# Kernel tuning notes

Measured on AMD Instinct MI355X. Metric: run time of the kernel, lower is better.

## Reference

```python
import jax, jax.numpy as jnp
import numpy as np

B, T, H = 32, 2048, 1024


def setup_inputs() -> dict:
    key = jax.random.key(0)
    ks = jax.random.split(key, 5)
    s = 1.0 / np.sqrt(H)
    return {
        "x": jax.random.normal(ks[0], (B, H), dtype=jnp.float32),
        "context": jax.random.normal(ks[1], (B, T, H), dtype=jnp.float32),
        "mask": jnp.ones((B, T), dtype=bool),
        "Wq": jax.random.normal(ks[2], (H, H), dtype=jnp.float32) * s,
        "bq": jnp.zeros((H,), dtype=jnp.float32),
        "Wm": jax.random.normal(ks[3], (H, H), dtype=jnp.float32) * s,
        "bm": jnp.zeros((H,), dtype=jnp.float32),
        "v": jax.random.normal(ks[4], (H,), dtype=jnp.float32) * s,
    }


def reference(x, context, mask, Wq, bq, Wm, bm, v):
    # h_x: [B,1,H]; h_c: [B,T,H]  (mask is unused, matching the original module)
    h_x = (x @ Wq.T + bq)[:, None, :]
    h_c = jnp.einsum('bth,oh->bto', context, Wm) + bm
    # score: [B,T] = tanh(h_x + h_c) . v, then softmax over T
    score = jax.nn.softmax(jnp.einsum('bth,h->bt', jnp.tanh(h_x + h_c), v), axis=-1)
    # context-weighted sum over T -> [B,H]
    c = jnp.einsum('bth,bt->bh', context, score)
    return (c, score)
```

## Files before the change

### kernel.cpp

```cpp
#include <hip/hip_runtime.h>
#include <math.h>

#define B_ 32
#define T_ 2048
#define H_ 1024

typedef __bf16 bf16x8 __attribute__((ext_vector_type(8)));
typedef float f32x4 __attribute__((ext_vector_type(4)));

__device__ __forceinline__ unsigned short f2bf(float f) {
  unsigned int u = __float_as_uint(f);
  u += 0x7fffu + ((u >> 16) & 1u);
  return (unsigned short)(u >> 16);
}

__device__ __forceinline__ float bf2f(unsigned short s) {
  return __uint_as_float(((unsigned int)s) << 16);
}

__device__ __forceinline__ float fast_tanh(float x) {
  float e = __expf(2.0f * x);
  return 1.0f - __fdividef(2.0f, e + 1.0f);
}

__device__ __forceinline__ void async16(const void* g, void* l) {
  typedef const __attribute__((address_space(1))) void* gvp;
  typedef __attribute__((address_space(3))) void* lvp;
  __builtin_amdgcn_global_load_lds((gvp)(unsigned long long)g,
                                   (lvp)(unsigned int)(unsigned long long)l,
                                   16, 0, 0);
}

__global__ void prep_kernel(const float* __restrict__ x, const float* __restrict__ Wq,
                            const float* __restrict__ bq, const float* __restrict__ bm,
                            const float* __restrict__ Wm, const float* __restrict__ ctx,
                            float* __restrict__ hxb, unsigned short* __restrict__ wmb,
                            unsigned short* __restrict__ ctxb,
                            float* __restrict__ logits, float* __restrict__ outc) {
  int blk = blockIdx.x, tid = threadIdx.x;
  if (blk < 8192) {
    int wave = tid >> 6, lane = tid & 63;
    int pair = (blk << 2) + wave;
    int b = pair >> 10, o = pair & (H_ - 1);
    const float4* wr = (const float4*)(Wq + (size_t)o * H_);
    const float4* xr = (const float4*)(x + (size_t)b * H_);
    float s = 0.f;
#pragma unroll
    for (int s4 = 0; s4 < 4; ++s4) {
      float4 wv = wr[(s4 << 6) + lane];
      float4 xv = xr[(s4 << 6) + lane];
      s += wv.x * xv.x + wv.y * xv.y + wv.z * xv.z + wv.w * xv.w;
    }
#pragma unroll
    for (int d = 1; d < 64; d <<= 1) s += __shfl_xor(s, d);
    if (lane == 0) hxb[(b << 10) + o] = s + bq[o] + bm[o];
  } else if (blk < 9216) {
    int i = ((blk - 8192) << 10) + (tid << 2);
    float4 wv = *(const float4*)(Wm + i);
    *(ushort4*)(wmb + i) = make_ushort4(f2bf(wv.x), f2bf(wv.y), f2bf(wv.z), f2bf(wv.w));
  } else if (blk < 9312) {
    int zblk = blk - 9216;
    if (zblk < 64) {
      *(float4*)(logits + (zblk << 10) + (tid << 2)) = (float4){0.f, 0.f, 0.f, 0.f};
    } else {
      *(float4*)(outc + ((zblk - 64) << 10) + (tid << 2)) = (float4){0.f, 0.f, 0.f, 0.f};
    }
  } else {
    size_t i = ((size_t)(blk - 9312) << 11) + ((size_t)tid << 3);
    float4 a = *(const float4*)(ctx + i);
    float4 c = *(const float4*)(ctx + i + 4);
    *(ushort4*)(ctxb + i) = make_ushort4(f2bf(a.x), f2bf(a.y), f2bf(a.z), f2bf(a.w));
    *(ushort4*)(ctxb + i + 4) = make_ushort4(f2bf(c.x), f2bf(c.y), f2bf(c.z), f2bf(c.w));
  }
}

template <bool PRECONV>
__global__ __launch_bounds__(256) void score_kernel(
    const float* __restrict__ ctxf, const unsigned short* __restrict__ ctxb,
    const unsigned short* __restrict__ wmb,
    const float* __restrict__ hxb, const float* __restrict__ v,
    float* logits) {
  __shared__ __align__(16) unsigned short As[128 * 64];
  __shared__ __align__(16) unsigned short Bs[128 * 64];
  __shared__ float part[128];

  int tid = threadIdx.x;
  int xx = blockIdx.x;
  int ot = xx >> 9;
  int bt = xx & 511;
  int b = bt >> 4;
  int t0 = (bt & 15) << 7;
  int o0 = ot << 7;
  if (tid < 128) part[tid] = 0.f;

  int lane = tid & 63;
  int wave = tid >> 6;
  int wm = (wave >> 1) << 6;
  int wn = (wave & 1) << 6;
  int q = lane >> 4;
  int m = lane & 15;

  const unsigned short* cb = PRECONV ? (ctxb + ((size_t)b * T_ + t0) * H_) : nullptr;
  const float* cf = PRECONV ? nullptr : (ctxf + ((size_t)b * T_ + t0) * H_);
  const unsigned short* wb = wmb + (size_t)o0 * H_;

  f32x4 acc[4][4];
#pragma unroll
  for (int i = 0; i < 4; ++i)
#pragma unroll
    for (int j = 0; j < 4; ++j) acc[i][j] = (f32x4){0.f, 0.f, 0.f, 0.f};

  for (int k0 = 0; k0 < H_; k0 += 64) {
    __syncthreads();
#pragma unroll
    for (int i = 0; i < 4; ++i) {
      int ig = (wave << 2) + i;
      int p = (ig << 6) + lane;
      int row = p >> 3;
      int gl = (p & 7) ^ (row & 7);
      size_t goff = (size_t)row * H_ + k0 + (gl << 3);
      if (PRECONV) {
        async16(cb + goff, (char*)As + ((size_t)ig << 10));
      } else {
        int arow = (tid >> 3) + (i << 5);
        int agl = tid & 7;
        int agp = agl ^ (arow & 7);
        const float* src = cf + (size_t)arow * H_ + k0 + (agl << 3);
        float4 f0 = *(const float4*)(src);
        float4 f1 = *(const float4*)(src + 4);
        unsigned short* dst = As + (arow << 6) + (agp << 3);
        *(ushort4*)(dst) = make_ushort4(f2bf(f0.x), f2bf(f0.y), f2bf(f0.z), f2bf(f0.w));
        *(ushort4*)(dst + 4) = make_ushort4(f2bf(f1.x), f2bf(f1.y), f2bf(f1.z), f2bf(f1.w));
      }
      async16(wb + goff, (char*)Bs + ((size_t)ig << 10));
    }
    __syncthreads();
#pragma unroll
    for (int kk = 0; kk < 2; ++kk) {
      bf16x8 af[4], bfr[4];
#pragma unroll
      for (int i = 0; i < 4; ++i) {
        int row = wm + (i << 4) + m;
        int gp = ((kk << 2) + q) ^ (row & 7);
        af[i] = *(const bf16x8*)(As + (row << 6) + (gp << 3));
      }
#pragma unroll
      for (int j = 0; j < 4; ++j) {
        int row = wn + (j << 4) + m;
        int gp = ((kk << 2) + q) ^ (row & 7);
        bfr[j] = *(const bf16x8*)(Bs + (row << 6) + (gp << 3));
      }
#pragma unroll
      for (int i = 0; i < 4; ++i)
#pragma unroll
        for (int j = 0; j < 4; ++j)
          acc[i][j] = __builtin_amdgcn_mfma_f32_16x16x32_bf16(af[i], bfr[j], acc[i][j], 0, 0, 0);
    }
  }

  float hb[4], vv[4];
#pragma unroll
  for (int j = 0; j < 4; ++j) {
    int o = o0 + wn + (j << 4) + m;
    hb[j] = hxb[(b << 10) + o];
    vv[j] = v[o];
  }
#pragma unroll
  for (int i = 0; i < 4; ++i) {
#pragma unroll
    for (int r = 0; r < 4; ++r) {
      float s = 0.f;
#pragma unroll
      for (int j = 0; j < 4; ++j) s += fast_tanh(acc[i][j][r] + hb[j]) * vv[j];
      s += __shfl_xor(s, 1);
      s += __shfl_xor(s, 2);
      s += __shfl_xor(s, 4);
      s += __shfl_xor(s, 8);
      if (m == 0) atomicAdd(&part[wm + (i << 4) + (q << 2) + r], s);
    }
  }
  __syncthreads();
  if (tid < 128) atomicAdd(&logits[b * T_ + t0 + tid], part[tid]);
}

template <bool PRECONV>
__global__ void wsum_kernel(const float* __restrict__ ctxf, const unsigned short* __restrict__ ctxb,
                            const float* __restrict__ logits,
                            float* __restrict__ score, float* __restrict__ outc) {
  int tid = threadIdx.x;
  int b = blockIdx.y;
  int tc = blockIdx.x << 7;
  __shared__ float wred[4];
  __shared__ float sc[128];

  const float* lb = logits + b * T_;
  float l[8];
  float mx = -3.4e38f;
#pragma unroll
  for (int i = 0; i < 8; ++i) { l[i] = lb[tid + (i << 8)]; mx = fmaxf(mx, l[i]); }
#pragma unroll
  for (int d = 1; d < 64; d <<= 1) mx = fmaxf(mx, __shfl_xor(mx, d));
  if ((tid & 63) == 0) wred[tid >> 6] = mx;
  __syncthreads();
  mx = fmaxf(fmaxf(wred[0], wred[1]), fmaxf(wred[2], wred[3]));
  __syncthreads();
  float e[8];
  float se = 0.f;
#pragma unroll
  for (int i = 0; i < 8; ++i) { e[i] = __expf(l[i] - mx); se += e[i]; }
#pragma unroll
  for (int d = 1; d < 64; d <<= 1) se += __shfl_xor(se, d);
  if ((tid & 63) == 0) wred[tid >> 6] = se;
  __syncthreads();
  se = wred[0] + wred[1] + wred[2] + wred[3];
  float inv = 1.0f / se;
#pragma unroll
  for (int i = 0; i < 8; ++i) {
    int tg = tid + (i << 8);
    if ((tg >> 7) == (int)blockIdx.x) sc[tg & 127] = e[i] * inv;
  }
  if (blockIdx.x == 0) {
#pragma unroll
    for (int i = 0; i < 8; ++i) score[b * T_ + tid + (i << 8)] = e[i] * inv;
  }
  __syncthreads();

  int h = tid << 2;
  float s0 = 0.f, s1 = 0.f, s2 = 0.f, s3 = 0.f;
  if (PRECONV) {
    const unsigned short* cp = ctxb + ((size_t)b * T_ + tc) * H_ + h;
#pragma unroll 4
    for (int t = 0; t < 128; ++t) {
      uint2 u = *(const uint2*)(cp + (size_t)t * H_);
      float w = sc[t];
      s0 += bf2f((unsigned short)(u.x & 0xffffu)) * w;
      s1 += bf2f((unsigned short)(u.x >> 16)) * w;
      s2 += bf2f((unsigned short)(u.y & 0xffffu)) * w;
      s3 += bf2f((unsigned short)(u.y >> 16)) * w;
    }
  } else {
    const float* cp = ctxf + ((size_t)b * T_ + tc) * H_ + h;
#pragma unroll 4
    for (int t = 0; t < 128; ++t) {
      float4 f = *(const float4*)(cp + (size_t)t * H_);
      float w = sc[t];
      s0 += f.x * w; s1 += f.y * w; s2 += f.z * w; s3 += f.w * w;
    }
  }
  float* op = outc + (b << 10) + h;
  atomicAdd(op + 0, s0);
  atomicAdd(op + 1, s1);
  atomicAdd(op + 2, s2);
  atomicAdd(op + 3, s3);
}

extern "C" void kernel_launch(void* const* d_in, const int* in_sizes, int n_in,
                              void* d_out, int out_size, void* d_ws, size_t ws_size,
                              hipStream_t stream) {
  const float* x   = (const float*)d_in[0];
  const float* ctx = (const float*)d_in[1];
  const float* Wq  = (const float*)d_in[3];
  const float* bq  = (const float*)d_in[4];
  const float* Wm  = (const float*)d_in[5];
  const float* bm  = (const float*)d_in[6];
  const float* v   = (const float*)d_in[7];

  float* out_c = (float*)d_out;
  float* out_s = out_c + B_ * H_;

  char* ws = (char*)d_ws;
  float* hxb = (float*)ws;
  unsigned short* wmb = (unsigned short*)(ws + 131072);
  float* logits = (float*)(ws + 131072 + 2097152);
  size_t off_ctxb = 131072 + 2097152 + 262144;
  unsigned short* ctxb = (unsigned short*)(ws + off_ctxb);
  size_t need = off_ctxb + (size_t)B_ * T_ * H_ * 2;
  bool preconv = (ws_size >= need);

  int prep_blocks = preconv ? (9312 + 32768) : 9312;
  prep_kernel<<<dim3(prep_blocks), 256, 0, stream>>>(x, Wq, bq, bm, Wm, ctx, hxb, wmb,
                                                     preconv ? ctxb : nullptr, logits, out_c);
  if (preconv) {
    score_kernel<true><<<dim3(4096), 256, 0, stream>>>(ctx, ctxb, wmb, hxb, v, logits);
    wsum_kernel<true><<<dim3(T_ / 128, B_), 256, 0, stream>>>(ctx, ctxb, logits, out_s, out_c);
  } else {
    score_kernel<false><<<dim3(4096), 256, 0, stream>>>(ctx, ctxb, wmb, hxb, v, logits);
    wsum_kernel<false><<<dim3(T_ / 128, B_), 256, 0, stream>>>(ctx, ctxb, logits, out_s, out_c);
  }
}
```

Baseline: 653.8 us.

## Fuse softmax and weighted context sum into the score GEMM kernel

Each score block now loops over all eight 128-wide output chunks itself, so the full logit for its 128 timesteps is ready on-chip. The block then applies an unnormalised exp (without max subtraction) and accumulates the exp-weighted context sum straight away, while its context rows are likely still in cache. Global sums are collected by atomics, and a small finalize kernel divides by the per-batch denominator. This removes the logits round trip, the separate wsum kernel and its cross-block softmax recompute. The hx GEMV also now reuses each Wq row across all batches. In exchange the grid drops from 4096 to 512 blocks, which lowers parallelism and latency hiding, and dropping the max subtraction risks overflow if logits grow large.

```diff
diff --git a/kernel.cpp b/kernel.cpp
--- a/kernel.cpp
+++ b/kernel.cpp
@@ -36,37 +36,39 @@
                             const float* __restrict__ Wm, const float* __restrict__ ctx,
                             float* __restrict__ hxb, unsigned short* __restrict__ wmb,
                             unsigned short* __restrict__ ctxb,
-                            float* __restrict__ logits, float* __restrict__ outc) {
+                            float* __restrict__ den, float* __restrict__ outc) {
   int blk = blockIdx.x, tid = threadIdx.x;
-  if (blk < 8192) {
+  if (blk < 256) {
     int wave = tid >> 6, lane = tid & 63;
-    int pair = (blk << 2) + wave;
-    int b = pair >> 10, o = pair & (H_ - 1);
+    int o = (blk << 2) + wave;
     const float4* wr = (const float4*)(Wq + (size_t)o * H_);
-    const float4* xr = (const float4*)(x + (size_t)b * H_);
-    float s = 0.f;
-#pragma unroll
-    for (int s4 = 0; s4 < 4; ++s4) {
-      float4 wv = wr[(s4 << 6) + lane];
-      float4 xv = xr[(s4 << 6) + lane];
-      s += wv.x * xv.x + wv.y * xv.y + wv.z * xv.z + wv.w * xv.w;
-    }
-#pragma unroll
-    for (int d = 1; d < 64; d <<= 1) s += __shfl_xor(s, d);
-    if (lane == 0) hxb[(b << 10) + o] = s + bq[o] + bm[o];
-  } else if (blk < 9216) {
-    int i = ((blk - 8192) << 10) + (tid << 2);
+    float4 wv[4];
+#pragma unroll
+    for (int s4 = 0; s4 < 4; ++s4) wv[s4] = wr[(s4 << 6) + lane];
+    float bias = bq[o] + bm[o];
+#pragma unroll 4
+    for (int b = 0; b < B_; ++b) {
+      const float4* xr = (const float4*)(x + (size_t)b * H_);
+      float s = 0.f;
+#pragma unroll
+      for (int s4 = 0; s4 < 4; ++s4) {
+        float4 xv = xr[(s4 << 6) + lane];
+        s += wv[s4].x * xv.x + wv[s4].y * xv.y + wv[s4].z * xv.z + wv[s4].w * xv.w;
+      }
+#pragma unroll
+      for (int d = 1; d < 64; d <<= 1) s += __shfl_xor(s, d);
+      if (lane == 0) hxb[(b << 10) + o] = s + bias;
+    }
+  } else if (blk < 1280) {
+    int i = ((blk - 256) << 10) + (tid << 2);
     float4 wv = *(const float4*)(Wm + i);
     *(ushort4*)(wmb + i) = make_ushort4(f2bf(wv.x), f2bf(wv.y), f2bf(wv.z), f2bf(wv.w));
-  } else if (blk < 9312) {
-    int zblk = blk - 9216;
-    if (zblk < 64) {
-      *(float4*)(logits + (zblk << 10) + (tid << 2)) = (float4){0.f, 0.f, 0.f, 0.f};
-    } else {
-      *(float4*)(outc + ((zblk - 64) << 10) + (tid << 2)) = (float4){0.f, 0.f, 0.f, 0.f};
-    }
+  } else if (blk < 1312) {
+    int zb = blk - 1280;
+    *(float4*)(outc + (zb << 10) + (tid << 2)) = (float4){0.f, 0.f, 0.f, 0.f};
+    if (zb == 0 && tid < B_) den[tid] = 0.f;
   } else {
-    size_t i = ((size_t)(blk - 9312) << 11) + ((size_t)tid << 3);
+    size_t i = ((size_t)(blk - 1312) << 11) + ((size_t)tid << 3);
     float4 a = *(const float4*)(ctx + i);
     float4 c = *(const float4*)(ctx + i + 4);
     *(ushort4*)(ctxb + i) = make_ushort4(f2bf(a.x), f2bf(a.y), f2bf(a.z), f2bf(a.w));
@@ -79,18 +81,16 @@
     const float* __restrict__ ctxf, const unsigned short* __restrict__ ctxb,
     const unsigned short* __restrict__ wmb,
     const float* __restrict__ hxb, const float* __restrict__ v,
-    float* logits) {
+    float* __restrict__ outs, float* __restrict__ outc, float* __restrict__ den) {
   __shared__ __align__(16) unsigned short As[128 * 64];
   __shared__ __align__(16) unsigned short Bs[128 * 64];
   __shared__ float part[128];
 
   int tid = threadIdx.x;
-  int xx = blockIdx.x;
-  int ot = xx >> 9;
-  int bt = xx & 511;
-  int b = bt >> 4;
-  int t0 = (bt & 15) << 7;
-  int o0 = ot << 7;
+  int bx = blockIdx.x;
+  int b = bx >> 4;
+  int t0 = (bx & 15) << 7;
+
   if (tid < 128) part[tid] = 0.f;
 
   int lane = tid & 63;
@@ -102,148 +102,120 @@
 
   const unsigned short* cb = PRECONV ? (ctxb + ((size_t)b * T_ + t0) * H_) : nullptr;
   const float* cf = PRECONV ? nullptr : (ctxf + ((size_t)b * T_ + t0) * H_);
-  const unsigned short* wb = wmb + (size_t)o0 * H_;
-
-  f32x4 acc[4][4];
-#pragma unroll
-  for (int i = 0; i < 4; ++i)
-#pragma unroll
-    for (int j = 0; j < 4; ++j) acc[i][j] = (f32x4){0.f, 0.f, 0.f, 0.f};
-
-  for (int k0 = 0; k0 < H_; k0 += 64) {
-    __syncthreads();
+
+  for (int oc = 0; oc < 8; ++oc) {
+    int o0 = oc << 7;
+    const unsigned short* wb = wmb + (size_t)o0 * H_;
+
+    f32x4 acc[4][4];
+#pragma unroll
+    for (int i = 0; i < 4; ++i)
+#pragma unroll
+      for (int j = 0; j < 4; ++j) acc[i][j] = (f32x4){0.f, 0.f, 0.f, 0.f};
+
+    for (int k0 = 0; k0 < H_; k0 += 64) {
+      __syncthreads();
+#pragma unroll
+      for (int i = 0; i < 4; ++i) {
+        int ig = (wave << 2) + i;
+        int p = (ig << 6) + lane;
+        int row = p >> 3;
+        int gl = (p & 7) ^ (row & 7);
+        size_t goff = (size_t)row * H_ + k0 + (gl << 3);
+        if (PRECONV) {
+          async16(cb + goff, (char*)As + ((size_t)ig << 10));
+        } else {
+          int arow = (tid >> 3) + (i << 5);
+          int agl = tid & 7;
+          int agp = agl ^ (arow & 7);
+          const float* src = cf + (size_t)arow * H_ + k0 + (agl << 3);
+          float4 f0 = *(const float4*)(src);
+          float4 f1 = *(const float4*)(src + 4);
+          unsigned short* dst = As + (arow << 6) + (agp << 3);
+          *(ushort4*)(dst) = make_ushort4(f2bf(f0.x), f2bf(f0.y), f2bf(f0.z), f2bf(f0.w));
+          *(ushort4*)(dst + 4) = make_ushort4(f2bf(f1.x), f2bf(f1.y), f2bf(f1.z), f2bf(f1.w));
+        }
+        async16(wb + goff, (char*)Bs + ((size_t)ig << 10));
+      }
+      __syncthreads();
+#pragma unroll
+      for (int kk = 0; kk < 2; ++kk) {
+        bf16x8 af[4], bfr[4];
+#pragma unroll
+        for (int i = 0; i < 4; ++i) {
+          int row = wm + (i << 4) + m;
+          int gp = ((kk << 2) + q) ^ (row & 7);
+          af[i] = *(const bf16x8*)(As + (row << 6) + (gp << 3));
+        }
+#pragma unroll
+        for (int j = 0; j < 4; ++j) {
+          int row = wn + (j << 4) + m;
+          int gp = ((kk << 2) + q) ^ (row & 7);
+          bfr[j] = *(const bf16x8*)(Bs + (row << 6) + (gp << 3));
+        }
+#pragma unroll
+        for (int i = 0; i < 4; ++i)
+#pragma unroll
+          for (int j = 0; j < 4; ++j)
+            acc[i][j] = __builtin_amdgcn_mfma_f32_16x16x32_bf16(af[i], bfr[j], acc[i][j], 0, 0, 0);
+      }
+    }
+
+    float hb[4], vv[4];
+#pragma unroll
+    for (int j = 0; j < 4; ++j) {
+      int o = o0 + wn + (j << 4) + m;
+      hb[j] = hxb[(b << 10) + o];
+      vv[j] = v[o];
+    }
 #pragma unroll
     for (int i = 0; i < 4; ++i) {
-      int ig = (wave << 2) + i;
-      int p = (ig << 6) + lane;
-      int row = p >> 3;
-      int gl = (p & 7) ^ (row & 7);
-      size_t goff = (size_t)row * H_ + k0 + (gl << 3);
-      if (PRECONV) {
-        async16(cb + goff, (char*)As + ((size_t)ig << 10));
-      } else {
-        int arow = (tid >> 3) + (i << 5);
-        int agl = tid & 7;
-        int agp = agl ^ (arow & 7);
-        const float* src = cf + (size_t)arow * H_ + k0 + (agl << 3);
-        float4 f0 = *(const float4*)(src);
-        float4 f1 = *(const float4*)(src + 4);
-        unsigned short* dst = As + (arow << 6) + (agp << 3);
-        *(ushort4*)(dst) = make_ushort4(f2bf(f0.x), f2bf(f0.y), f2bf(f0.z), f2bf(f0.w));
-        *(ushort4*)(dst + 4) = make_ushort4(f2bf(f1.x), f2bf(f1.y), f2bf(f1.z), f2bf(f1.w));
-      }
-      async16(wb + goff, (char*)Bs + ((size_t)ig << 10));
-    }
-    __syncthreads();
-#pragma unroll
-    for (int kk = 0; kk < 2; ++kk) {
-      bf16x8 af[4], bfr[4];
-#pragma unroll
-      for (int i = 0; i < 4; ++i) {
-        int row = wm + (i << 4) + m;
-        int gp = ((kk << 2) + q) ^ (row & 7);
-        af[i] = *(const bf16x8*)(As + (row << 6) + (gp << 3));
-      }
-#pragma unroll
-      for (int j = 0; j < 4; ++j) {
-        int row = wn + (j << 4) + m;
-        int gp = ((kk << 2) + q) ^ (row & 7);
-        bfr[j] = *(const bf16x8*)(Bs + (row << 6) + (gp << 3));
-      }
-#pragma unroll
-      for (int i = 0; i < 4; ++i)
-#pragma unroll
-        for (int j = 0; j < 4; ++j)
-          acc[i][j] = __builtin_amdgcn_mfma_f32_16x16x32_bf16(af[i], bfr[j], acc[i][j], 0, 0, 0);
-    }
-  }
-
-  float hb[4], vv[4];
-#pragma unroll
-  for (int j = 0; j < 4; ++j) {
-    int o = o0 + wn + (j << 4) + m;
-    hb[j] = hxb[(b << 10) + o];
-    vv[j] = v[o];
-  }
-#pragma unroll
-  for (int i = 0; i < 4; ++i) {
-#pragma unroll
-    for (int r = 0; r < 4; ++r) {
-      float s = 0.f;
-#pragma unroll
-      for (int j = 0; j < 4; ++j) s += fast_tanh(acc[i][j][r] + hb[j]) * vv[j];
-      s += __shfl_xor(s, 1);
-      s += __shfl_xor(s, 2);
-      s += __shfl_xor(s, 4);
-      s += __shfl_xor(s, 8);
-      if (m == 0) atomicAdd(&part[wm + (i << 4) + (q << 2) + r], s);
-    }
-  }
+#pragma unroll
+      for (int r = 0; r < 4; ++r) {
+        float s = 0.f;
+#pragma unroll
+        for (int j = 0; j < 4; ++j) s += fast_tanh(acc[i][j][r] + hb[j]) * vv[j];
+        s += __shfl_xor(s, 1);
+        s += __shfl_xor(s, 2);
+        s += __shfl_xor(s, 4);
+        s += __shfl_xor(s, 8);
+        if (m == 0) atomicAdd(&part[wm + (i << 4) + (q << 2) + r], s);
+      }
+    }
+  }
+
   __syncthreads();
-  if (tid < 128) atomicAdd(&logits[b * T_ + t0 + tid], part[tid]);
-}
-
-template <bool PRECONV>
-__global__ void wsum_kernel(const float* __restrict__ ctxf, const unsigned short* __restrict__ ctxb,
-                            const float* __restrict__ logits,
-                            float* __restrict__ score, float* __restrict__ outc) {
-  int tid = threadIdx.x;
-  int b = blockIdx.y;
-  int tc = blockIdx.x << 7;
-  __shared__ float wred[4];
-  __shared__ float sc[128];
-
-  const float* lb = logits + b * T_;
-  float l[8];
-  float mx = -3.4e38f;
-#pragma unroll
-  for (int i = 0; i < 8; ++i) { l[i] = lb[tid + (i << 8)]; mx = fmaxf(mx, l[i]); }
-#pragma unroll
-  for (int d = 1; d < 64; d <<= 1) mx = fmaxf(mx, __shfl_xor(mx, d));
-  if ((tid & 63) == 0) wred[tid >> 6] = mx;
-  __syncthreads();
-  mx = fmaxf(fmaxf(wred[0], wred[1]), fmaxf(wred[2], wred[3]));
-  __syncthreads();
-  float e[8];
-  float se = 0.f;
-#pragma unroll
-  for (int i = 0; i < 8; ++i) { e[i] = __expf(l[i] - mx); se += e[i]; }
-#pragma unroll
-  for (int d = 1; d < 64; d <<= 1) se += __shfl_xor(se, d);
-  if ((tid & 63) == 0) wred[tid >> 6] = se;
-  __syncthreads();
-  se = wred[0] + wred[1] + wred[2] + wred[3];
-  float inv = 1.0f / se;
-#pragma unroll
-  for (int i = 0; i < 8; ++i) {
-    int tg = tid + (i << 8);
-    if ((tg >> 7) == (int)blockIdx.x) sc[tg & 127] = e[i] * inv;
-  }
-  if (blockIdx.x == 0) {
-#pragma unroll
-    for (int i = 0; i < 8; ++i) score[b * T_ + tid + (i << 8)] = e[i] * inv;
-  }
+  float e = 0.f;
+  if (tid < 128) {
+    e = __expf(part[tid]);
+    part[tid] = e;
+    outs[(size_t)b * T_ + t0 + tid] = e;
+  }
+  float es = e;
+#pragma unroll
+  for (int d = 1; d < 64; d <<= 1) es += __shfl_xor(es, d);
+  if (lane == 0) atomicAdd(&den[b], es);
   __syncthreads();
 
   int h = tid << 2;
   float s0 = 0.f, s1 = 0.f, s2 = 0.f, s3 = 0.f;
   if (PRECONV) {
-    const unsigned short* cp = ctxb + ((size_t)b * T_ + tc) * H_ + h;
+    const unsigned short* cp = cb + h;
 #pragma unroll 4
     for (int t = 0; t < 128; ++t) {
       uint2 u = *(const uint2*)(cp + (size_t)t * H_);
-      float w = sc[t];
+      float w = part[t];
       s0 += bf2f((unsigned short)(u.x & 0xffffu)) * w;
       s1 += bf2f((unsigned short)(u.x >> 16)) * w;
       s2 += bf2f((unsigned short)(u.y & 0xffffu)) * w;
       s3 += bf2f((unsigned short)(u.y >> 16)) * w;
     }
   } else {
-    const float* cp = ctxf + ((size_t)b * T_ + tc) * H_ + h;
+    const float* cp = cf + h;
 #pragma unroll 4
     for (int t = 0; t < 128; ++t) {
       float4 f = *(const float4*)(cp + (size_t)t * H_);
-      float w = sc[t];
+      float w = part[t];
       s0 += f.x * w; s1 += f.y * w; s2 += f.z * w; s3 += f.w * w;
     }
   }
@@ -252,6 +224,16 @@
   atomicAdd(op + 1, s1);
   atomicAdd(op + 2, s2);
   atomicAdd(op + 3, s3);
+}
+
+__global__ void finalize_kernel(float* __restrict__ outc, float* __restrict__ outs,
+                                const float* __restrict__ den) {
+  int b = blockIdx.x, tid = threadIdx.x;
+  float inv = 1.0f / den[b];
+#pragma unroll
+  for (int i = 0; i < 4; ++i) outc[(b << 10) + tid + (i << 8)] *= inv;
+#pragma unroll
+  for (int i = 0; i < 8; ++i) outs[b * T_ + tid + (i << 8)] *= inv;
 }
 
 extern "C" void kernel_launch(void* const* d_in, const int* in_sizes, int n_in,
@@ -271,20 +253,19 @@
   char* ws = (char*)d_ws;
   float* hxb = (float*)ws;
   unsigned short* wmb = (unsigned short*)(ws + 131072);
-  float* logits = (float*)(ws + 131072 + 2097152);
+  float* den = (float*)(ws + 131072 + 2097152);
   size_t off_ctxb = 131072 + 2097152 + 262144;
   unsigned short* ctxb = (unsigned short*)(ws + off_ctxb);
   size_t need = off_ctxb + (size_t)B_ * T_ * H_ * 2;
   bool preconv = (ws_size >= need);
 
-  int prep_blocks = preconv ? (9312 + 32768) : 9312;
+  int prep_blocks = preconv ? (1312 + 32768) : 1312;
   prep_kernel<<<dim3(prep_blocks), 256, 0, stream>>>(x, Wq, bq, bm, Wm, ctx, hxb, wmb,
-                                                     preconv ? ctxb : nullptr, logits, out_c);
+                                                     preconv ? ctxb : nullptr, den, out_c);
   if (preconv) {
-    score_kernel<true><<<dim3(4096), 256, 0, stream>>>(ctx, ctxb, wmb, hxb, v, logits);
-    wsum_kernel<true><<<dim3(T_ / 128, B_), 256, 0, stream>>>(ctx, ctxb, logits, out_s, out_c);
+    score_kernel<true><<<dim3(512), 256, 0, stream>>>(ctx, ctxb, wmb, hxb, v, out_s, out_c, den);
   } else {
-    score_kernel<false><<<dim3(4096), 256, 0, stream>>>(ctx, ctxb, wmb, hxb, v, logits);
-    wsum_kernel<false><<<dim3(T_ / 128, B_), 256, 0, stream>>>(ctx, ctxb, logits, out_s, out_c);
-  }
-}
+    score_kernel<false><<<dim3(512), 256, 0, stream>>>(ctx, ctxb, wmb, hxb, v, out_s, out_c, den);
+  }
+  finalize_kernel<<<dim3(B_), 256, 0, stream>>>(out_c, out_s, den);
+}
```

Result: slower. 834.8 us (+27.7%).

## Drop context pre-conversion pass and convert fp32 context inline in score kernel

Applied to the files above, without the earlier changes.

Removes the separate pass that converted the whole fp32 context tensor to bf16 in workspace. The score kernel now always loads fp32 context and converts it to bf16 while staging into shared memory. It also reorders the block index so the eight output-column tiles for the same context rows run adjacently and can share those rows in cache. The weighted-sum kernel reads fp32 context with smaller T chunks for more blocks. This saves a full read-write pass over context, at the cost of synchronous fp32 loads in the GEMM and twice the fp32 traffic in the weighted sum.

```diff
diff --git a/kernel.cpp b/kernel.cpp
--- a/kernel.cpp
+++ b/kernel.cpp
@@ -12,10 +12,6 @@
   unsigned int u = __float_as_uint(f);
   u += 0x7fffu + ((u >> 16) & 1u);
   return (unsigned short)(u >> 16);
-}
-
-__device__ __forceinline__ float bf2f(unsigned short s) {
-  return __uint_as_float(((unsigned int)s) << 16);
 }
 
 __device__ __forceinline__ float fast_tanh(float x) {
@@ -33,9 +29,8 @@
 
 __global__ void prep_kernel(const float* __restrict__ x, const float* __restrict__ Wq,
                             const float* __restrict__ bq, const float* __restrict__ bm,
-                            const float* __restrict__ Wm, const float* __restrict__ ctx,
+                            const float* __restrict__ Wm,
                             float* __restrict__ hxb, unsigned short* __restrict__ wmb,
-                            unsigned short* __restrict__ ctxb,
                             float* __restrict__ logits, float* __restrict__ outc) {
   int blk = blockIdx.x, tid = threadIdx.x;
   if (blk < 8192) {
@@ -58,39 +53,30 @@
     int i = ((blk - 8192) << 10) + (tid << 2);
     float4 wv = *(const float4*)(Wm + i);
     *(ushort4*)(wmb + i) = make_ushort4(f2bf(wv.x), f2bf(wv.y), f2bf(wv.z), f2bf(wv.w));
-  } else if (blk < 9312) {
-    int zblk = blk - 9216;
-    if (zblk < 64) {
-      *(float4*)(logits + (zblk << 10) + (tid << 2)) = (float4){0.f, 0.f, 0.f, 0.f};
-    } else {
-      *(float4*)(outc + ((zblk - 64) << 10) + (tid << 2)) = (float4){0.f, 0.f, 0.f, 0.f};
-    }
+  } else if (blk < 9280) {
+    int zb = blk - 9216;
+    *(float4*)(logits + (zb << 10) + (tid << 2)) = (float4){0.f, 0.f, 0.f, 0.f};
   } else {
-    size_t i = ((size_t)(blk - 9312) << 11) + ((size_t)tid << 3);
-    float4 a = *(const float4*)(ctx + i);
-    float4 c = *(const float4*)(ctx + i + 4);
-    *(ushort4*)(ctxb + i) = make_ushort4(f2bf(a.x), f2bf(a.y), f2bf(a.z), f2bf(a.w));
-    *(ushort4*)(ctxb + i + 4) = make_ushort4(f2bf(c.x), f2bf(c.y), f2bf(c.z), f2bf(c.w));
-  }
-}
-
-template <bool PRECONV>
+    int zb = blk - 9280;
+    *(float4*)(outc + (zb << 10) + (tid << 2)) = (float4){0.f, 0.f, 0.f, 0.f};
+  }
+}
+
 __global__ __launch_bounds__(256) void score_kernel(
-    const float* __restrict__ ctxf, const unsigned short* __restrict__ ctxb,
-    const unsigned short* __restrict__ wmb,
+    const float* __restrict__ ctx, const unsigned short* __restrict__ wmb,
     const float* __restrict__ hxb, const float* __restrict__ v,
-    float* logits) {
+    float* __restrict__ logits) {
   __shared__ __align__(16) unsigned short As[128 * 64];
   __shared__ __align__(16) unsigned short Bs[128 * 64];
   __shared__ float part[128];
 
   int tid = threadIdx.x;
-  int xx = blockIdx.x;
-  int ot = xx >> 9;
-  int bt = xx & 511;
-  int b = bt >> 4;
-  int t0 = (bt & 15) << 7;
-  int o0 = ot << 7;
+  int bx = blockIdx.x;
+  int g = bx >> 3;
+  int oc = bx & 7;
+  int b = g >> 4;
+  int t0 = (g & 15) << 7;
+  int o0 = oc << 7;
   if (tid < 128) part[tid] = 0.f;
 
   int lane = tid & 63;
@@ -100,8 +86,7 @@
   int q = lane >> 4;
   int m = lane & 15;
 
-  const unsigned short* cb = PRECONV ? (ctxb + ((size_t)b * T_ + t0) * H_) : nullptr;
-  const float* cf = PRECONV ? nullptr : (ctxf + ((size_t)b * T_ + t0) * H_);
+  const float* cf = ctx + ((size_t)b * T_ + t0) * H_;
   const unsigned short* wb = wmb + (size_t)o0 * H_;
 
   f32x4 acc[4][4];
@@ -119,20 +104,16 @@
       int row = p >> 3;
       int gl = (p & 7) ^ (row & 7);
       size_t goff = (size_t)row * H_ + k0 + (gl << 3);
-      if (PRECONV) {
-        async16(cb + goff, (char*)As + ((size_t)ig << 10));
-      } else {
-        int arow = (tid >> 3) + (i << 5);
-        int agl = tid & 7;
-        int agp = agl ^ (arow & 7);
-        const float* src = cf + (size_t)arow * H_ + k0 + (agl << 3);
-        float4 f0 = *(const float4*)(src);
-        float4 f1 = *(const float4*)(src + 4);
-        unsigned short* dst = As + (arow << 6) + (agp << 3);
-        *(ushort4*)(dst) = make_ushort4(f2bf(f0.x), f2bf(f0.y), f2bf(f0.z), f2bf(f0.w));
-        *(ushort4*)(dst + 4) = make_ushort4(f2bf(f1.x), f2bf(f1.y), f2bf(f1.z), f2bf(f1.w));
-      }
       async16(wb + goff, (char*)Bs + ((size_t)ig << 10));
+      int arow = (tid >> 3) + (i << 5);
+      int agl = tid & 7;
+      int agp = agl ^ (arow & 7);
+      const float* src = cf + (size_t)arow * H_ + k0 + (agl << 3);
+      float4 f0 = *(const float4*)(src);
+      float4 f1 = *(const float4*)(src + 4);
+      unsigned short* dst = As + (arow << 6) + (agp << 3);
+      *(ushort4*)(dst) = make_ushort4(f2bf(f0.x), f2bf(f0.y), f2bf(f0.z), f2bf(f0.w));
+      *(ushort4*)(dst + 4) = make_ushort4(f2bf(f1.x), f2bf(f1.y), f2bf(f1.z), f2bf(f1.w));
     }
     __syncthreads();
 #pragma unroll
@@ -183,15 +164,14 @@
   if (tid < 128) atomicAdd(&logits[b * T_ + t0 + tid], part[tid]);
 }
 
-template <bool PRECONV>
-__global__ void wsum_kernel(const float* __restrict__ ctxf, const unsigned short* __restrict__ ctxb,
+__global__ void wsum_kernel(const float* __restrict__ ctx,
                             const float* __restrict__ logits,
                             float* __restrict__ score, float* __restrict__ outc) {
   int tid = threadIdx.x;
   int b = blockIdx.y;
-  int tc = blockIdx.x << 7;
+  int tc = blockIdx.x << 6;
   __shared__ float wred[4];
-  __shared__ float sc[128];
+  __shared__ float sc[64];
 
   const float* lb = logits + b * T_;
   float l[8];
@@ -217,7 +197,7 @@
 #pragma unroll
   for (int i = 0; i < 8; ++i) {
     int tg = tid + (i << 8);
-    if ((tg >> 7) == (int)blockIdx.x) sc[tg & 127] = e[i] * inv;
+    if ((tg >> 6) == (int)blockIdx.x) sc[tg & 63] = e[i] * inv;
   }
   if (blockIdx.x == 0) {
 #pragma unroll
@@ -226,26 +206,13 @@
   __syncthreads();
 
   int h = tid << 2;
+  const float* cp = ctx + ((size_t)b * T_ + tc) * H_ + h;
   float s0 = 0.f, s1 = 0.f, s2 = 0.f, s3 = 0.f;
-  if (PRECONV) {
-    const unsigned short* cp = ctxb + ((size_t)b * T_ + tc) * H_ + h;
 #pragma unroll 4
-    for (int t = 0; t < 128; ++t) {
-      uint2 u = *(const uint2*)(cp + (size_t)t * H_);
-      float w = sc[t];
-      s0 += bf2f((unsigned short)(u.x & 0xffffu)) * w;
-      s1 += bf2f((unsigned short)(u.x >> 16)) * w;
-      s2 += bf2f((unsigned short)(u.y & 0xffffu)) * w;
-      s3 += bf2f((unsigned short)(u.y >> 16)) * w;
-    }
-  } else {
-    const float* cp = ctxf + ((size_t)b * T_ + tc) * H_ + h;
-#pragma unroll 4
-    for (int t = 0; t < 128; ++t) {
-      float4 f = *(const float4*)(cp + (size_t)t * H_);
-      float w = sc[t];
-      s0 += f.x * w; s1 += f.y * w; s2 += f.z * w; s3 += f.w * w;
-    }
+  for (int t = 0; t < 64; ++t) {
+    float4 f = *(const float4*)(cp + (size_t)t * H_);
+    float w = sc[t];
+    s0 += f.x * w; s1 += f.y * w; s2 += f.z * w; s3 += f.w * w;
   }
   float* op = outc + (b << 10) + h;
   atomicAdd(op + 0, s0);
@@ -272,19 +239,9 @@
   float* hxb = (float*)ws;
   unsigned short* wmb = (unsigned short*)(ws + 131072);
   float* logits = (float*)(ws + 131072 + 2097152);
-  size_t off_ctxb = 131072 + 2097152 + 262144;
-  unsigned short* ctxb = (unsigned short*)(ws + off_ctxb);
-  size_t need = off_ctxb + (size_t)B_ * T_ * H_ * 2;
-  bool preconv = (ws_size >= need);
-
-  int prep_blocks = preconv ? (9312 + 32768) : 9312;
-  prep_kernel<<<dim3(prep_blocks), 256, 0, stream>>>(x, Wq, bq, bm, Wm, ctx, hxb, wmb,
-                                                     preconv ? ctxb : nullptr, logits, out_c);
-  if (preconv) {
-    score_kernel<true><<<dim3(4096), 256, 0, stream>>>(ctx, ctxb, wmb, hxb, v, logits);
-    wsum_kernel<true><<<dim3(T_ / 128, B_), 256, 0, stream>>>(ctx, ctxb, logits, out_s, out_c);
-  } else {
-    score_kernel<false><<<dim3(4096), 256, 0, stream>>>(ctx, ctxb, wmb, hxb, v, logits);
-    wsum_kernel<false><<<dim3(T_ / 128, B_), 256, 0, stream>>>(ctx, ctxb, logits, out_s, out_c);
-  }
-}
+
+  prep_kernel<<<dim3(9312), 256, 0, stream>>>(x, Wq, bq, bm, Wm, hxb, wmb,
+                                              logits, out_c);
+  score_kernel<<<dim3(4096), 256, 0, stream>>>(ctx, wmb, hxb, v, logits);
+  wsum_kernel<<<dim3(T_ / 64, B_), 256, 0, stream>>>(ctx, logits, out_s, out_c);
+}
```

Measured after the change: 706.5 us. 8.1% more time.
